# Kernel optimization log

Hardware: AMD Instinct MI355X
Metric: run time of the kernel (lower is better)

Reference implementation:

```python
import jax, jax.numpy as jnp
import numpy as np

# e3nn normalize2mom gain for tanh (1/sqrt(E[tanh(z)^2]), z~N(0,1))
TANH_GAIN = 1.5927116870880127
B, M_IN, M_HID, M_OUT = 8192, 64, 128, 64

_W_SPECS = {
    'b1_l1_w0': (64, 64), 'b1_l1_w1': (64, 64), 'b1_l2_w0': (64, 64), 'b1_l2_w1': (64, 64),
    'b1_tp_ss': (64, 64, 128), 'b1_tp_vv': (64, 64, 128), 'b1_tp_sv': (64, 64, 128), 'b1_tp_vs': (64, 64, 128),
    'b1_g_ws': (128, 128), 'b1_g_wg': (128, 128), 'b1_g_wv': (128, 128),
    'b1_o_w0': (128, 128), 'b1_o_w1': (128, 128),
    'b2_l1_w0': (128, 128), 'b2_l1_w1': (128, 128), 'b2_l2_w0': (128, 128), 'b2_l2_w1': (128, 128),
    'b2_tp_ss': (128, 128, 128), 'b2_tp_vv': (128, 128, 128), 'b2_tp_sv': (128, 128, 128), 'b2_tp_vs': (128, 128, 128),
    'b2_g_ws': (128, 128), 'b2_g_wg': (128, 128), 'b2_g_wv': (128, 128),
    'b2_o_w0': (128, 128), 'b2_o_w1': (128, 128),
    'f_w0': (128, 64), 'f_w1': (128, 64),
}


def setup_inputs() -> dict:
    key = jax.random.key(0)
    ks = jax.random.split(key, len(_W_SPECS) + 1)
    d = {'x': jax.random.normal(ks[0], (B, M_IN + 3 * M_IN), jnp.float32)}
    for i, (name, shp) in enumerate(_W_SPECS.items()):
        d[name] = jax.random.normal(ks[i + 1], shp, jnp.float32)  # e3nn weights ~ N(0,1)
    return d


def _lin(s, v, w0, w1):
    # o3.Linear on 'Mx0e+Mx1o': per-irrep block matmul, path_normalization='element' -> 1/sqrt(fan_in)
    c = 1.0 / np.sqrt(w0.shape[0])
    return (s @ w0) * c, jnp.einsum('bui,uw->bwi', v, w1) * c


def _tp(s1, v1, s2, v2, wss, wvv, wsv, wvs):
    # FullyConnectedTensorProduct, irrep_normalization='component', path_normalization='element'.
    # Two uvw paths feed each output irrep -> path_weight = sqrt(dim_out / (2*M*M)).
    # CG values: w3j(0,0,0)=1; w3j(0,1,1)=delta/sqrt(3); w3j(1,0,1)=delta/sqrt(3); w3j(1,1,0)=delta/sqrt(3).
    M = s1.shape[-1]
    c = 1.0 / (M * np.sqrt(2.0))
    s = c * jnp.einsum('bu,bv,uvw->bw', s1, s2, wss) \
        + (c / np.sqrt(3.0)) * jnp.einsum('bui,bvi,uvw->bw', v1, v2, wvv)
    v = c * (jnp.einsum('bu,bvi,uvw->bwi', s1, v2, wsv)
             + jnp.einsum('bui,bv,uvw->bwi', v1, s2, wvs))
    return s, v


def _gate(s, v, ws, wg, wv):
    # LearnableGate: o3.Linear to (scalars | gate scalars | vectors), then e3nn Gate
    # (tanh w/ normalize2mom gain on scalars and gates; elementwise gate*vector has unit path weight).
    c = 1.0 / np.sqrt(ws.shape[0])
    sl = (s @ ws) * c
    g = (s @ wg) * c
    vl = jnp.einsum('bui,uw->bwi', v, wv) * c
    return TANH_GAIN * jnp.tanh(sl), (TANH_GAIN * jnp.tanh(g))[..., None] * vl


def _block(s, v, p):
    l1w0, l1w1, l2w0, l2w1, wss, wvv, wsv, wvs, gws, gwg, gwv, ow0, ow1 = p
    s1, v1 = _lin(s, v, l1w0, l1w1)
    s2, v2 = _lin(s, v, l2w0, l2w1)
    s, v = _tp(s1, v1, s2, v2, wss, wvv, wsv, wvs)
    s, v = _gate(s, v, gws, gwg, gwv)
    return _lin(s, v, ow0, ow1)


def _forward(x, *w):
    s = x[:, :M_IN]
    v = x[:, M_IN:].reshape(x.shape[0], M_IN, 3)
    s, v = _block(s, v, w[0:13])
    s, v = _block(s, v, w[13:26])
    s, v = _lin(s, v, w[26], w[27])
    return jnp.concatenate([s, v.reshape(v.shape[0], -1)], axis=-1)


def reference(x, b1_l1_w0, b1_l1_w1, b1_l2_w0, b1_l2_w1, b1_tp_ss, b1_tp_vv, b1_tp_sv, b1_tp_vs, b1_g_ws, b1_g_wg, b1_g_wv, b1_o_w0, b1_o_w1, b2_l1_w0, b2_l1_w1, b2_l2_w0, b2_l2_w1, b2_tp_ss, b2_tp_vv, b2_tp_sv, b2_tp_vs, b2_g_ws, b2_g_wg, b2_g_wv, b2_o_w0, b2_o_w1, f_w0, f_w1):
    return _forward(x, b1_l1_w0, b1_l1_w1, b1_l2_w0, b1_l2_w1, b1_tp_ss, b1_tp_vv, b1_tp_sv, b1_tp_vs, b1_g_ws, b1_g_wg, b1_g_wv, b1_o_w0, b1_o_w1, b2_l1_w0, b2_l1_w1, b2_l2_w0, b2_l2_w1, b2_tp_ss, b2_tp_vv, b2_tp_sv, b2_tp_vs, b2_g_ws, b2_g_wg, b2_g_wv, b2_o_w0, b2_o_w1, f_w0, f_w1)
```

## Files before the change

kernel.cpp:

```cpp
#include <hip/hip_runtime.h>
#include <math.h>

typedef _Float16 f16;
typedef __attribute__((ext_vector_type(8))) _Float16 half8;
typedef __attribute__((ext_vector_type(4))) _Float16 half4;
typedef __attribute__((ext_vector_type(4))) float floatx4;

#define NB 8192

struct ConvJob { const float* src; f16* dst; int K; int N; int ucount; float scale; int swz; };
struct ConvJobs { ConvJob j[28]; };

__global__ void convert_w(ConvJobs JJ) {
    ConvJob jb = JJ.j[blockIdx.z];
    int u = blockIdx.x;
    if (u >= jb.ucount) return;
    __shared__ f16 tile[128 * 136];
    const int K = jb.K, N = jb.N;
    const int npad = N + 8;
    const int nsh = (N == 128) ? 7 : 6;
    const int ksh = (K == 128) ? 7 : 6;
    const float* src = jb.src + (size_t)u * K * N;
    for (int idx = threadIdx.x; idx < K * N; idx += 256) {
        int k = idx >> nsh, n = idx & (N - 1);
        tile[k * npad + n] = (f16)(src[idx] * jb.scale);
    }
    __syncthreads();
    f16* dst = jb.dst + (size_t)u * N * K;
    for (int idx = threadIdx.x; idx < N * K; idx += 256) {
        int n = idx >> ksh, rem = idx & (K - 1);
        int g2 = rem >> 3, jj = rem & 7;
        int g = jb.swz ? (g2 ^ (n & jb.swz)) : g2;
        int k = g * 8 + jj;
        dst[idx] = tile[k * npad + n];
    }
}

__global__ void x_to_planes(const float* __restrict__ x, f16* s_p, f16* v0, f16* v1, f16* v2) {
    int t = blockIdx.x * 256 + threadIdx.x;
    if (t >= NB * 64) return;
    int b = t >> 6, u = t & 63;
    const float* xr = x + (size_t)b * 256;
    s_p[t] = (f16)xr[u];
    v0[t] = (f16)xr[64 + 3 * u + 0];
    v1[t] = (f16)xr[64 + 3 * u + 1];
    v2[t] = (f16)xr[64 + 3 * u + 2];
}

struct TpJob { const f16* p; const f16* q; const f16* w; float* out; int pstride; int qstride; };
struct TpJobs { TpJob j[10]; };

template <int M>
__launch_bounds__(256, (M == 128) ? 3 : 4)
__global__ void tp_unit(TpJobs JJ) {
    TpJob jb = JJ.j[blockIdx.z];
    constexpr int KC = M / 32;
    constexpr int GPR = M / 8;
    constexpr int GM = GPR - 1;
    constexpr int SLABH = 64 * M;
    constexpr int PIECES = SLABH / 8;
    constexpr int IPW = PIECES / 256;
    constexpr int SLABFULL = 128 * M;
    __shared__ f16 w_lds[2][SLABH];
    const int tid = threadIdx.x, lane = tid & 63, wave = tid >> 6;
    const int wm = wave & 1, wn = wave >> 1;
    const int l15 = lane & 15, quad = lane >> 4;
    const int rowBase = blockIdx.x * 128;
    const int colBase = blockIdx.y * 64;

    half8 qf[4][KC];
    int prow[4];
    #pragma unroll
    for (int t = 0; t < 4; t++) {
        int row = rowBase + wm * 64 + t * 16 + l15;
        prow[t] = row;
        const f16* qr = jb.q + (size_t)row * jb.qstride;
        #pragma unroll
        for (int c = 0; c < KC; c++) qf[t][c] = *(const half8*)(qr + c * 32 + quad * 8);
    }
    floatx4 acc[4][2];
    #pragma unroll
    for (int a = 0; a < 4; a++)
        #pragma unroll
        for (int b = 0; b < 2; b++) acc[a][b] = (floatx4){0.f, 0.f, 0.f, 0.f};

    int rd_off[2][KC];
    #pragma unroll
    for (int nt = 0; nt < 2; nt++) {
        int nl = wn * 32 + nt * 16 + l15;
        #pragma unroll
        for (int c = 0; c < KC; c++) {
            int g = c * 4 + quad;
            rd_off[nt][c] = nl * M + ((g ^ (nl & GM)) << 3);
        }
    }

    const int wpBase = wave * (PIECES / 4);
    const f16* wsrc0 = jb.w + (size_t)colBase * M + (size_t)(wpBase + lane) * 8;
    f16* ldst0 = &w_lds[0][0] + (size_t)wpBase * 8;
    f16* ldst1 = &w_lds[1][0] + (size_t)wpBase * 8;
    auto stage = [&](int u, int buf) {
        const f16* src = wsrc0 + (size_t)u * SLABFULL;
        f16* dst = buf ? ldst1 : ldst0;
        #pragma unroll
        for (int i = 0; i < IPW; i++) {
            __builtin_amdgcn_global_load_lds(
                (const __attribute__((address_space(1))) void*)(src + i * 64 * 8),
                (__attribute__((address_space(3))) void*)(dst + i * 64 * 8),
                16, 0, 0);
        }
    };

    stage(0, 0);
    __syncthreads();

    for (int uc = 0; uc < M / 8; uc++) {
        half8 pcur[4];
        #pragma unroll
        for (int t = 0; t < 4; t++)
            pcur[t] = *(const half8*)(jb.p + (size_t)prow[t] * jb.pstride + uc * 8);
        #pragma unroll
        for (int j = 0; j < 8; j++) {
            const int u = uc * 8 + j;
            const int cur = j & 1;
            if (j != 7 || uc != M / 8 - 1) stage(u + 1, cur ^ 1);
            #pragma unroll
            for (int c = 0; c < KC; c++) {
                half8 af[4];
                #pragma unroll
                for (int t = 0; t < 4; t++) {
                    f16 pv = pcur[t][j];
                    half8 p8 = {pv, pv, pv, pv, pv, pv, pv, pv};
                    af[t] = qf[t][c] * p8;
                }
                #pragma unroll
                for (int nt = 0; nt < 2; nt++) {
                    half8 bf = *(const half8*)&w_lds[cur][rd_off[nt][c]];
                    #pragma unroll
                    for (int t = 0; t < 4; t++)
                        acc[t][nt] = __builtin_amdgcn_mfma_f32_16x16x32_f16(af[t], bf, acc[t][nt], 0, 0, 0);
                }
            }
            __syncthreads();
        }
    }
    #pragma unroll
    for (int t = 0; t < 4; t++)
        #pragma unroll
        for (int nt = 0; nt < 2; nt++) {
            int col = colBase + wn * 32 + nt * 16 + l15;
            float* orow = jb.out + (size_t)(rowBase + wm * 64 + t * 16 + quad * 4) * 128 + col;
            #pragma unroll
            for (int r = 0; r < 4; r++) orow[(size_t)r * 128] = acc[t][nt][r];
        }
}

struct SmallJob { const f16* A; const f16* W; char* out; int astride; int ostride;
                  int ocol; int cstride; int mode; int Njob; int ny;
                  const f16* Amul; int mstride; };
struct SmallJobs { SmallJob j[4]; };

template <int K>
__launch_bounds__(256, 2)
__global__ void small_gemm(SmallJobs JJ) {
    SmallJob jb = JJ.j[blockIdx.z];
    if ((int)blockIdx.y >= jb.ny) return;
    constexpr int KC = K / 32;
    constexpr int NP = K + 8;
    constexpr int PR = K / 8;
    constexpr int PPT = 128 * K / 8 / 256;
    __shared__ f16 w_lds[128 * NP];
    const int tid = threadIdx.x, lane = tid & 63, wave = tid >> 6;
    const int wm = wave & 1, wn = wave >> 1;
    const int l15 = lane & 15, quad = lane >> 4;
    const int rowBase = blockIdx.x * 128;
    const int nBase = blockIdx.y * 128;

    #pragma unroll
    for (int t = 0; t < PPT; t++) {
        int idx = t * 256 + tid;
        int r = idx / PR, pc = idx % PR;
        int4 v = {0, 0, 0, 0};
        if (nBase + r < jb.Njob)
            v = *(const int4*)(jb.W + (size_t)(nBase + r) * K + pc * 8);
        *(int4*)&w_lds[r * NP + pc * 8] = v;
    }
    half8 qf[4][KC];
    for (int t = 0; t < 4; t++) {
        int row = rowBase + wm * 64 + t * 16 + l15;
        const f16* ar = jb.A + (size_t)row * jb.astride;
        #pragma unroll
        for (int c = 0; c < KC; c++) qf[t][c] = *(const half8*)(ar + c * 32 + quad * 8);
        if (jb.Amul) {
            const f16* mr = jb.Amul + (size_t)row * jb.mstride;
            #pragma unroll
            for (int c = 0; c < KC; c++) qf[t][c] = qf[t][c] * *(const half8*)(mr + c * 32 + quad * 8);
        }
    }
    floatx4 acc[4][4];
    #pragma unroll
    for (int a = 0; a < 4; a++)
        #pragma unroll
        for (int b = 0; b < 4; b++) acc[a][b] = (floatx4){0.f, 0.f, 0.f, 0.f};
    __syncthreads();
    #pragma unroll
    for (int c = 0; c < KC; c++)
        #pragma unroll
        for (int nt = 0; nt < 4; nt++) {
            half8 bf = *(const half8*)&w_lds[(wn * 64 + nt * 16 + l15) * NP + c * 32 + quad * 8];
            #pragma unroll
            for (int t = 0; t < 4; t++)
                acc[t][nt] = __builtin_amdgcn_mfma_f32_16x16x32_f16(qf[t][c], bf, acc[t][nt], 0, 0, 0);
        }
    const float GAIN = 1.5927116870880127f;
    #pragma unroll
    for (int t = 0; t < 4; t++)
        #pragma unroll
        for (int nt = 0; nt < 4; nt++) {
            int col = nBase + wn * 64 + nt * 16 + l15;
            if (col >= jb.Njob) continue;
            int rowB = rowBase + wm * 64 + t * 16 + quad * 4;
            #pragma unroll
            for (int r = 0; r < 4; r++) {
                float v = acc[t][nt][r];
                size_t ro = (size_t)(rowB + r) * jb.ostride;
                if (jb.mode == 0)      ((f16*)jb.out)[ro + jb.ocol + col] = (f16)v;
                else if (jb.mode == 1) ((f16*)jb.out)[ro + jb.ocol + col] = (f16)(GAIN * tanhf(v));
                else                   ((float*)jb.out)[ro + jb.ocol + (size_t)col * jb.cstride] = v;
            }
        }
}

__global__ void tp_reduce(const float4* __restrict__ P, half4* s_tp, half4* v0, half4* v1, half4* v2) {
    int t = blockIdx.x * 256 + threadIdx.x;
    if (t >= NB * 32) return;
    const size_t S = (size_t)NB * 32;
    float4 a0 = P[t], a1 = P[S + t], a2 = P[2 * S + t], a3 = P[3 * S + t];
    float4 b0 = P[4 * S + t], b1 = P[5 * S + t], b2 = P[6 * S + t];
    float4 c0 = P[7 * S + t], c1 = P[8 * S + t], c2 = P[9 * S + t];
    s_tp[t] = (half4){(f16)(a0.x + a1.x + a2.x + a3.x), (f16)(a0.y + a1.y + a2.y + a3.y),
                      (f16)(a0.z + a1.z + a2.z + a3.z), (f16)(a0.w + a1.w + a2.w + a3.w)};
    v0[t] = (half4){(f16)(b0.x + c0.x), (f16)(b0.y + c0.y), (f16)(b0.z + c0.z), (f16)(b0.w + c0.w)};
    v1[t] = (half4){(f16)(b1.x + c1.x), (f16)(b1.y + c1.y), (f16)(b1.z + c1.z), (f16)(b1.w + c1.w)};
    v2[t] = (half4){(f16)(b2.x + c2.x), (f16)(b2.y + c2.y), (f16)(b2.z + c2.z), (f16)(b2.w + c2.w)};
}

extern "C" void kernel_launch(void* const* d_in, const int* in_sizes, int n_in,
                              void* d_out, int out_size, void* d_ws, size_t ws_size,
                              hipStream_t stream) {
    const float* x = (const float*)d_in[0];
    const float* W_IN[28];
    for (int i = 0; i < 28; i++) W_IN[i] = (const float*)d_in[1 + i];

    char* base = (char*)d_ws;
    size_t off = 0;
    auto alloc = [&](size_t bytes) -> char* {
        char* p = base + off;
        off += (bytes + 255) & ~(size_t)255;
        return p;
    };
    const size_t S128 = (size_t)NB * 128;

    f16* Wl12_b1_s = (f16*)alloc(8192 * 2);
    f16* Wl12_b1_v = (f16*)alloc(8192 * 2);
    f16* Wl12_b2_s = (f16*)alloc(32768 * 2);
    f16* Wl12_b2_v = (f16*)alloc(32768 * 2);
    f16* Wtp_b1[4]; for (int i = 0; i < 4; i++) Wtp_b1[i] = (f16*)alloc((size_t)64 * 128 * 64 * 2);
    f16* Wtp_b2[4]; for (int i = 0; i < 4; i++) Wtp_b2[i] = (f16*)alloc((size_t)128 * 128 * 128 * 2);
    f16* Wg_b1_sg = (f16*)alloc(32768 * 2);
    f16* Wg_b1_v  = (f16*)alloc(16384 * 2);
    f16* Wg_b2_sg = (f16*)alloc(32768 * 2);
    f16* Wg_b2_v  = (f16*)alloc(16384 * 2);
    f16* Wo_b1_s = (f16*)alloc(16384 * 2);
    f16* Wo_b1_v = (f16*)alloc(16384 * 2);
    f16* Wo_b2_s = (f16*)alloc(16384 * 2);
    f16* Wo_b2_v = (f16*)alloc(16384 * 2);
    f16* Wf_s = (f16*)alloc(8192 * 2);
    f16* Wf_v = (f16*)alloc(8192 * 2);
    f16* s_p = (f16*)alloc((size_t)NB * 64 * 2);
    f16* v_p[3]; for (int i = 0; i < 3; i++) v_p[i] = (f16*)alloc((size_t)NB * 64 * 2);
    f16* Breg = (f16*)alloc((size_t)4 * NB * 256 * 2);
    float* Part = (float*)alloc((size_t)10 * S128 * 4);
    f16* Dreg = (f16*)alloc((size_t)4 * S128 * 2);
    f16* Ereg = (f16*)alloc((size_t)5 * S128 * 2);
    f16* Freg = (f16*)alloc((size_t)4 * S128 * 2);
    (void)ws_size; (void)in_sizes; (void)n_in; (void)out_size;

    const float c_l1 = 0.125f;
    const float c128 = 0.088388347648318447f;
    const float c1 = 1.0f / (64.0f * 1.4142135623730951f);
    const float c2 = 1.0f / (128.0f * 1.4142135623730951f);
    const float i3 = 0.57735026918962584f;

    ConvJobs CJ;
    int jn = 0;
    auto CV = [&](const float* s, f16* d, int K, int N, int uc, float sc, int swz) {
        CJ.j[jn++] = ConvJob{s, d, K, N, uc, sc, swz};
    };
    CV(W_IN[0], Wl12_b1_s, 64, 64, 1, c_l1, 0);  CV(W_IN[2], Wl12_b1_s + 4096, 64, 64, 1, c_l1, 0);
    CV(W_IN[1], Wl12_b1_v, 64, 64, 1, c_l1, 0);  CV(W_IN[3], Wl12_b1_v + 4096, 64, 64, 1, c_l1, 0);
    CV(W_IN[13], Wl12_b2_s, 128, 128, 1, c128, 0); CV(W_IN[15], Wl12_b2_s + 16384, 128, 128, 1, c128, 0);
    CV(W_IN[14], Wl12_b2_v, 128, 128, 1, c128, 0); CV(W_IN[16], Wl12_b2_v + 16384, 128, 128, 1, c128, 0);
    CV(W_IN[4], Wtp_b1[0], 64, 128, 64, c1, 7);  CV(W_IN[5], Wtp_b1[1], 64, 128, 64, c1 * i3, 7);
    CV(W_IN[6], Wtp_b1[2], 64, 128, 64, c1, 7);  CV(W_IN[7], Wtp_b1[3], 64, 128, 64, c1, 7);
    CV(W_IN[17], Wtp_b2[0], 128, 128, 128, c2, 15); CV(W_IN[18], Wtp_b2[1], 128, 128, 128, c2 * i3, 15);
    CV(W_IN[19], Wtp_b2[2], 128, 128, 128, c2, 15); CV(W_IN[20], Wtp_b2[3], 128, 128, 128, c2, 15);
    CV(W_IN[8], Wg_b1_sg, 128, 128, 1, c128, 0);  CV(W_IN[9], Wg_b1_sg + 16384, 128, 128, 1, c128, 0);
    CV(W_IN[10], Wg_b1_v, 128, 128, 1, c128, 0);
    CV(W_IN[21], Wg_b2_sg, 128, 128, 1, c128, 0); CV(W_IN[22], Wg_b2_sg + 16384, 128, 128, 1, c128, 0);
    CV(W_IN[23], Wg_b2_v, 128, 128, 1, c128, 0);
    CV(W_IN[11], Wo_b1_s, 128, 128, 1, c128, 0);  CV(W_IN[12], Wo_b1_v, 128, 128, 1, c128, 0);
    CV(W_IN[24], Wo_b2_s, 128, 128, 1, c128, 0);  CV(W_IN[25], Wo_b2_v, 128, 128, 1, c128, 0);
    CV(W_IN[26], Wf_s, 128, 64, 1, c128, 0);      CV(W_IN[27], Wf_v, 128, 64, 1, c128, 0);
    convert_w<<<dim3(128, 1, 28), 256, 0, stream>>>(CJ);

    x_to_planes<<<NB * 64 / 256, 256, 0, stream>>>(x, s_p, v_p[0], v_p[1], v_p[2]);

    auto SJ = [](const f16* A, const f16* W, void* out, int as, int os, int oc, int cs,
                 int mode, int Nj, int ny, const f16* Amul, int ms) {
        return SmallJob{A, W, (char*)out, as, os, oc, cs, mode, Nj, ny, Amul, ms};
    };

    f16* s12 = Breg;
    f16* v12[3]; for (int i = 0; i < 3; i++) v12[i] = Breg + (size_t)(1 + i) * NB * 128;
    f16* s_tp = Dreg; f16* v_tp[3]; for (int i = 0; i < 3; i++) v_tp[i] = Dreg + (1 + i) * S128;
    f16* sg_gg = Ereg;
    f16* vl[3]; for (int i = 0; i < 3; i++) vl[i] = Ereg + 2 * S128 + i * S128;
    f16* s_o = Freg; f16* v_o[3]; for (int i = 0; i < 3; i++) v_o[i] = Freg + (1 + i) * S128;

    {
        SmallJobs J;
        J.j[0] = SJ(s_p, Wl12_b1_s, s12, 64, 128, 0, 1, 0, 128, 1, nullptr, 0);
        for (int i = 0; i < 3; i++) J.j[1 + i] = SJ(v_p[i], Wl12_b1_v, v12[i], 64, 128, 0, 1, 0, 128, 1, nullptr, 0);
        small_gemm<64><<<dim3(64, 1, 4), 256, 0, stream>>>(J);
    }
    {
        TpJobs J;
        J.j[0] = TpJob{s12, s12 + 64, Wtp_b1[0], Part + 0 * S128, 128, 128};
        for (int i = 0; i < 3; i++) J.j[1 + i] = TpJob{v12[i], v12[i] + 64, Wtp_b1[1], Part + (1 + i) * S128, 128, 128};
        for (int i = 0; i < 3; i++) J.j[4 + i] = TpJob{s12, v12[i] + 64, Wtp_b1[2], Part + (4 + i) * S128, 128, 128};
        for (int i = 0; i < 3; i++) J.j[7 + i] = TpJob{v12[i], s12 + 64, Wtp_b1[3], Part + (7 + i) * S128, 128, 128};
        tp_unit<64><<<dim3(64, 2, 10), 256, 0, stream>>>(J);
    }
    tp_reduce<<<NB * 32 / 256, 256, 0, stream>>>((const float4*)Part, (half4*)s_tp, (half4*)v_tp[0], (half4*)v_tp[1], (half4*)v_tp[2]);
    {
        SmallJobs J;
        J.j[0] = SJ(s_tp, Wg_b1_sg, sg_gg, 128, 256, 0, 1, 1, 256, 2, nullptr, 0);
        for (int i = 0; i < 3; i++) J.j[1 + i] = SJ(v_tp[i], Wg_b1_v, vl[i], 128, 128, 0, 1, 0, 128, 1, nullptr, 0);
        small_gemm<128><<<dim3(64, 2, 4), 256, 0, stream>>>(J);
    }
    {
        SmallJobs J;
        J.j[0] = SJ(sg_gg, Wo_b1_s, s_o, 256, 128, 0, 1, 0, 128, 1, nullptr, 0);
        for (int i = 0; i < 3; i++) J.j[1 + i] = SJ(vl[i], Wo_b1_v, v_o[i], 128, 128, 0, 1, 0, 128, 1, sg_gg + 128, 256);
        small_gemm<128><<<dim3(64, 1, 4), 256, 0, stream>>>(J);
    }
    f16* s12b = Breg;
    f16* v12b[3]; for (int i = 0; i < 3; i++) v12b[i] = Breg + (size_t)(1 + i) * NB * 256;
    {
        SmallJobs J;
        J.j[0] = SJ(s_o, Wl12_b2_s, s12b, 128, 256, 0, 1, 0, 256, 2, nullptr, 0);
        for (int i = 0; i < 3; i++) J.j[1 + i] = SJ(v_o[i], Wl12_b2_v, v12b[i], 128, 256, 0, 1, 0, 256, 2, nullptr, 0);
        small_gemm<128><<<dim3(64, 2, 4), 256, 0, stream>>>(J);
    }
    {
        TpJobs J;
        J.j[0] = TpJob{s12b, s12b + 128, Wtp_b2[0], Part + 0 * S128, 256, 256};
        for (int i = 0; i < 3; i++) J.j[1 + i] = TpJob{v12b[i], v12b[i] + 128, Wtp_b2[1], Part + (1 + i) * S128, 256, 256};
        for (int i = 0; i < 3; i++) J.j[4 + i] = TpJob{s12b, v12b[i] + 128, Wtp_b2[2], Part + (4 + i) * S128, 256, 256};
        for (int i = 0; i < 3; i++) J.j[7 + i] = TpJob{v12b[i], s12b + 128, Wtp_b2[3], Part + (7 + i) * S128, 256, 256};
        tp_unit<128><<<dim3(64, 2, 10), 256, 0, stream>>>(J);
    }
    tp_reduce<<<NB * 32 / 256, 256, 0, stream>>>((const float4*)Part, (half4*)s_tp, (half4*)v_tp[0], (half4*)v_tp[1], (half4*)v_tp[2]);
    {
        SmallJobs J;
        J.j[0] = SJ(s_tp, Wg_b2_sg, sg_gg, 128, 256, 0, 1, 1, 256, 2, nullptr, 0);
        for (int i = 0; i < 3; i++) J.j[1 + i] = SJ(v_tp[i], Wg_b2_v, vl[i], 128, 128, 0, 1, 0, 128, 1, nullptr, 0);
        small_gemm<128><<<dim3(64, 2, 4), 256, 0, stream>>>(J);
    }
    {
        SmallJobs J;
        J.j[0] = SJ(sg_gg, Wo_b2_s, s_o, 256, 128, 0, 1, 0, 128, 1, nullptr, 0);
        for (int i = 0; i < 3; i++) J.j[1 + i] = SJ(vl[i], Wo_b2_v, v_o[i], 128, 128, 0, 1, 0, 128, 1, sg_gg + 128, 256);
        small_gemm<128><<<dim3(64, 1, 4), 256, 0, stream>>>(J);
    }
    {
        SmallJobs J;
        J.j[0] = SJ(s_o, Wf_s, d_out, 128, 256, 0, 1, 2, 64, 1, nullptr, 0);
        for (int i = 0; i < 3; i++) J.j[1 + i] = SJ(v_o[i], Wf_v, d_out, 128, 256, 64 + i, 3, 2, 64, 1, nullptr, 0);
        small_gemm<128><<<dim3(64, 1, 4), 256, 0, stream>>>(J);
    }
}
```

Before: 638.3 us.

## Triple-buffer TP weight staging and fuse partial reduction into gate GEMM

The tensor-product kernel moves from double to triple LDS buffering. It prefetches two slabs ahead and replaces __syncthreads with a partial vmcnt wait plus barrier, so global-to-LDS loads can overlap compute. The separate tp_reduce kernel is removed, and the gate small_gemm now sums the fp32 partials directly while loading its A operand. This saves one launch and an fp16 intermediate round trip per block. In exchange the triple buffer raises LDS use, which may reduce occupancy for M=128, and the y=2 gate GEMM blocks re-read the fp32 partials redundantly.

```diff
diff --git a/kernel.cpp b/kernel.cpp
--- a/kernel.cpp
+++ b/kernel.cpp
@@ -61,7 +61,7 @@
     constexpr int PIECES = SLABH / 8;
     constexpr int IPW = PIECES / 256;
     constexpr int SLABFULL = 128 * M;
-    __shared__ f16 w_lds[2][SLABH];
+    __shared__ f16 w_lds[3][SLABH];
     const int tid = threadIdx.x, lane = tid & 63, wave = tid >> 6;
     const int wm = wave & 1, wn = wave >> 1;
     const int l15 = lane & 15, quad = lane >> 4;
@@ -97,11 +97,9 @@
 
     const int wpBase = wave * (PIECES / 4);
     const f16* wsrc0 = jb.w + (size_t)colBase * M + (size_t)(wpBase + lane) * 8;
-    f16* ldst0 = &w_lds[0][0] + (size_t)wpBase * 8;
-    f16* ldst1 = &w_lds[1][0] + (size_t)wpBase * 8;
     auto stage = [&](int u, int buf) {
         const f16* src = wsrc0 + (size_t)u * SLABFULL;
-        f16* dst = buf ? ldst1 : ldst0;
+        f16* dst = &w_lds[buf][0] + (size_t)wpBase * 8;
         #pragma unroll
         for (int i = 0; i < IPW; i++) {
             __builtin_amdgcn_global_load_lds(
@@ -112,8 +110,10 @@
     };
 
     stage(0, 0);
-    __syncthreads();
-
+    stage(1, 1);
+    __asm__ __volatile__("s_waitcnt vmcnt(%0)\n\ts_barrier" :: "n"(IPW) : "memory");
+
+    int ib = 0;
     for (int uc = 0; uc < M / 8; uc++) {
         half8 pcur[4];
         #pragma unroll
@@ -122,8 +122,9 @@
         #pragma unroll
         for (int j = 0; j < 8; j++) {
             const int u = uc * 8 + j;
-            const int cur = j & 1;
-            if (j != 7 || uc != M / 8 - 1) stage(u + 1, cur ^ 1);
+            int unext = u + 2; if (unext > M - 1) unext = M - 1;
+            int is = ib + 2; if (is >= 3) is -= 3;
+            stage(unext, is);
             #pragma unroll
             for (int c = 0; c < KC; c++) {
                 half8 af[4];
@@ -135,13 +136,14 @@
                 }
                 #pragma unroll
                 for (int nt = 0; nt < 2; nt++) {
-                    half8 bf = *(const half8*)&w_lds[cur][rd_off[nt][c]];
+                    half8 bf = *(const half8*)&w_lds[ib][rd_off[nt][c]];
                     #pragma unroll
                     for (int t = 0; t < 4; t++)
                         acc[t][nt] = __builtin_amdgcn_mfma_f32_16x16x32_f16(af[t], bf, acc[t][nt], 0, 0, 0);
                 }
             }
-            __syncthreads();
+            __asm__ __volatile__("s_waitcnt vmcnt(%0)\n\ts_barrier" :: "n"(IPW) : "memory");
+            ib = ib + 1; if (ib == 3) ib = 0;
         }
     }
     #pragma unroll
@@ -157,7 +159,9 @@
 
 struct SmallJob { const f16* A; const f16* W; char* out; int astride; int ostride;
                   int ocol; int cstride; int mode; int Njob; int ny;
-                  const f16* Amul; int mstride; };
+                  const f16* Amul; int mstride;
+                  const float* red0; const float* red1; const float* red2; const float* red3;
+                  int nred; };
 struct SmallJobs { SmallJob j[4]; };
 
 template <int K>
@@ -188,9 +192,23 @@
     half8 qf[4][KC];
     for (int t = 0; t < 4; t++) {
         int row = rowBase + wm * 64 + t * 16 + l15;
-        const f16* ar = jb.A + (size_t)row * jb.astride;
-        #pragma unroll
-        for (int c = 0; c < KC; c++) qf[t][c] = *(const half8*)(ar + c * 32 + quad * 8);
+        if (jb.nred) {
+            #pragma unroll
+            for (int c = 0; c < KC; c++) {
+                size_t boff = (size_t)row * 128 + c * 32 + quad * 8;
+                floatx4 s0 = *(const floatx4*)(jb.red0 + boff);
+                floatx4 s1 = *(const floatx4*)(jb.red0 + boff + 4);
+                if (jb.nred > 1) { s0 += *(const floatx4*)(jb.red1 + boff); s1 += *(const floatx4*)(jb.red1 + boff + 4); }
+                if (jb.nred > 2) { s0 += *(const floatx4*)(jb.red2 + boff); s1 += *(const floatx4*)(jb.red2 + boff + 4); }
+                if (jb.nred > 3) { s0 += *(const floatx4*)(jb.red3 + boff); s1 += *(const floatx4*)(jb.red3 + boff + 4); }
+                qf[t][c] = (half8){(f16)s0.x, (f16)s0.y, (f16)s0.z, (f16)s0.w,
+                                   (f16)s1.x, (f16)s1.y, (f16)s1.z, (f16)s1.w};
+            }
+        } else {
+            const f16* ar = jb.A + (size_t)row * jb.astride;
+            #pragma unroll
+            for (int c = 0; c < KC; c++) qf[t][c] = *(const half8*)(ar + c * 32 + quad * 8);
+        }
         if (jb.Amul) {
             const f16* mr = jb.Amul + (size_t)row * jb.mstride;
             #pragma unroll
@@ -229,20 +247,6 @@
                 else                   ((float*)jb.out)[ro + jb.ocol + (size_t)col * jb.cstride] = v;
             }
         }
-}
-
-__global__ void tp_reduce(const float4* __restrict__ P, half4* s_tp, half4* v0, half4* v1, half4* v2) {
-    int t = blockIdx.x * 256 + threadIdx.x;
-    if (t >= NB * 32) return;
-    const size_t S = (size_t)NB * 32;
-    float4 a0 = P[t], a1 = P[S + t], a2 = P[2 * S + t], a3 = P[3 * S + t];
-    float4 b0 = P[4 * S + t], b1 = P[5 * S + t], b2 = P[6 * S + t];
-    float4 c0 = P[7 * S + t], c1 = P[8 * S + t], c2 = P[9 * S + t];
-    s_tp[t] = (half4){(f16)(a0.x + a1.x + a2.x + a3.x), (f16)(a0.y + a1.y + a2.y + a3.y),
-                      (f16)(a0.z + a1.z + a2.z + a3.z), (f16)(a0.w + a1.w + a2.w + a3.w)};
-    v0[t] = (half4){(f16)(b0.x + c0.x), (f16)(b0.y + c0.y), (f16)(b0.z + c0.z), (f16)(b0.w + c0.w)};
-    v1[t] = (half4){(f16)(b1.x + c1.x), (f16)(b1.y + c1.y), (f16)(b1.z + c1.z), (f16)(b1.w + c1.w)};
-    v2[t] = (half4){(f16)(b2.x + c2.x), (f16)(b2.y + c2.y), (f16)(b2.z + c2.z), (f16)(b2.w + c2.w)};
 }
 
 extern "C" void kernel_launch(void* const* d_in, const int* in_sizes, int n_in,
@@ -281,7 +285,6 @@
     f16* v_p[3]; for (int i = 0; i < 3; i++) v_p[i] = (f16*)alloc((size_t)NB * 64 * 2);
     f16* Breg = (f16*)alloc((size_t)4 * NB * 256 * 2);
     float* Part = (float*)alloc((size_t)10 * S128 * 4);
-    f16* Dreg = (f16*)alloc((size_t)4 * S128 * 2);
     f16* Ereg = (f16*)alloc((size_t)5 * S128 * 2);
     f16* Freg = (f16*)alloc((size_t)4 * S128 * 2);
     (void)ws_size; (void)in_sizes; (void)n_in; (void)out_size;
@@ -318,12 +321,12 @@
 
     auto SJ = [](const f16* A, const f16* W, void* out, int as, int os, int oc, int cs,
                  int mode, int Nj, int ny, const f16* Amul, int ms) {
-        return SmallJob{A, W, (char*)out, as, os, oc, cs, mode, Nj, ny, Amul, ms};
+        return SmallJob{A, W, (char*)out, as, os, oc, cs, mode, Nj, ny, Amul, ms,
+                        nullptr, nullptr, nullptr, nullptr, 0};
     };
 
     f16* s12 = Breg;
     f16* v12[3]; for (int i = 0; i < 3; i++) v12[i] = Breg + (size_t)(1 + i) * NB * 128;
-    f16* s_tp = Dreg; f16* v_tp[3]; for (int i = 0; i < 3; i++) v_tp[i] = Dreg + (1 + i) * S128;
     f16* sg_gg = Ereg;
     f16* vl[3]; for (int i = 0; i < 3; i++) vl[i] = Ereg + 2 * S128 + i * S128;
     f16* s_o = Freg; f16* v_o[3]; for (int i = 0; i < 3; i++) v_o[i] = Freg + (1 + i) * S128;
@@ -342,11 +345,13 @@
         for (int i = 0; i < 3; i++) J.j[7 + i] = TpJob{v12[i], s12 + 64, Wtp_b1[3], Part + (7 + i) * S128, 128, 128};
         tp_unit<64><<<dim3(64, 2, 10), 256, 0, stream>>>(J);
     }
-    tp_reduce<<<NB * 32 / 256, 256, 0, stream>>>((const float4*)Part, (half4*)s_tp, (half4*)v_tp[0], (half4*)v_tp[1], (half4*)v_tp[2]);
-    {
-        SmallJobs J;
-        J.j[0] = SJ(s_tp, Wg_b1_sg, sg_gg, 128, 256, 0, 1, 1, 256, 2, nullptr, 0);
-        for (int i = 0; i < 3; i++) J.j[1 + i] = SJ(v_tp[i], Wg_b1_v, vl[i], 128, 128, 0, 1, 0, 128, 1, nullptr, 0);
+    {
+        SmallJobs J;
+        J.j[0] = SmallJob{nullptr, Wg_b1_sg, (char*)sg_gg, 128, 256, 0, 1, 1, 256, 2, nullptr, 0,
+                          Part + 0 * S128, Part + 1 * S128, Part + 2 * S128, Part + 3 * S128, 4};
+        for (int i = 0; i < 3; i++)
+            J.j[1 + i] = SmallJob{nullptr, Wg_b1_v, (char*)vl[i], 128, 128, 0, 1, 0, 128, 1, nullptr, 0,
+                                  Part + (4 + i) * S128, Part + (7 + i) * S128, nullptr, nullptr, 2};
         small_gemm<128><<<dim3(64, 2, 4), 256, 0, stream>>>(J);
     }
     {
@@ -371,11 +376,13 @@
         for (int i = 0; i < 3; i++) J.j[7 + i] = TpJob{v12b[i], s12b + 128, Wtp_b2[3], Part + (7 + i) * S128, 256, 256};
         tp_unit<128><<<dim3(64, 2, 10), 256, 0, stream>>>(J);
     }
-    tp_reduce<<<NB * 32 / 256, 256, 0, stream>>>((const float4*)Part, (half4*)s_tp, (half4*)v_tp[0], (half4*)v_tp[1], (half4*)v_tp[2]);
-    {
-        SmallJobs J;
-        J.j[0] = SJ(s_tp, Wg_b2_sg, sg_gg, 128, 256, 0, 1, 1, 256, 2, nullptr, 0);
-        for (int i = 0; i < 3; i++) J.j[1 + i] = SJ(v_tp[i], Wg_b2_v, vl[i], 128, 128, 0, 1, 0, 128, 1, nullptr, 0);
+    {
+        SmallJobs J;
+        J.j[0] = SmallJob{nullptr, Wg_b2_sg, (char*)sg_gg, 128, 256, 0, 1, 1, 256, 2, nullptr, 0,
+                          Part + 0 * S128, Part + 1 * S128, Part + 2 * S128, Part + 3 * S128, 4};
+        for (int i = 0; i < 3; i++)
+            J.j[1 + i] = SmallJob{nullptr, Wg_b2_v, (char*)vl[i], 128, 128, 0, 1, 0, 128, 1, nullptr, 0,
+                                  Part + (4 + i) * S128, Part + (7 + i) * S128, nullptr, nullptr, 2};
         small_gemm<128><<<dim3(64, 2, 4), 256, 0, stream>>>(J);
     }
     {
```

After: 703.0 us. 10.1% more time.

## Share weight slabs across three planes per TP block and pre-sum vv paths

Applied to the files above, without the earlier changes.

Restructures the tensor-product kernel so each block processes three row planes (the three vector components, or three row chunks for the ss path) against one staged weight slab. This reuses each LDS weight slab three times instead of once and cuts redundant weight traffic. The vv path sums its three components in registers before storing, which shrinks the partial buffer from ten to eight planes and reduces tp_reduce reads. It raises register pressure, lowers occupancy through launch bounds, and adds clamped rows and early exits for the ss job's uneven row tiling.

```diff
diff --git a/kernel.cpp b/kernel.cpp
--- a/kernel.cpp
+++ b/kernel.cpp
@@ -47,16 +47,18 @@
     v2[t] = (f16)xr[64 + 3 * u + 2];
 }
 
-struct TpJob { const f16* p; const f16* q; const f16* w; float* out; int pstride; int qstride; };
-struct TpJobs { TpJob j[10]; };
+struct Tp3Job { const f16* q0; const f16* q1; const f16* q2;
+                const f16* p0; const f16* p1; const f16* p2;
+                const f16* w; float* o0; float* o1; float* o2;
+                int qs; int ps; int rowmul; int rowadd; int sum; };
+struct Tp3Jobs { Tp3Job j[4]; };
 
 template <int M>
-__launch_bounds__(256, (M == 128) ? 3 : 4)
-__global__ void tp_unit(TpJobs JJ) {
-    TpJob jb = JJ.j[blockIdx.z];
+__launch_bounds__(256, (M == 128) ? 2 : 3)
+__global__ void tp3(Tp3Jobs JJ) {
+    Tp3Job jb = JJ.j[blockIdx.z];
     constexpr int KC = M / 32;
-    constexpr int GPR = M / 8;
-    constexpr int GM = GPR - 1;
+    constexpr int GM = M / 8 - 1;
     constexpr int SLABH = 64 * M;
     constexpr int PIECES = SLABH / 8;
     constexpr int IPW = PIECES / 256;
@@ -65,24 +67,34 @@
     const int tid = threadIdx.x, lane = tid & 63, wave = tid >> 6;
     const int wm = wave & 1, wn = wave >> 1;
     const int l15 = lane & 15, quad = lane >> 4;
-    const int rowBase = blockIdx.x * 128;
+    const int bx = blockIdx.x;
+    if (jb.rowmul == 192 && bx * 192 >= NB) return;
     const int colBase = blockIdx.y * 64;
 
-    half8 qf[4][KC];
-    int prow[4];
-    #pragma unroll
-    for (int t = 0; t < 4; t++) {
-        int row = rowBase + wm * 64 + t * 16 + l15;
-        prow[t] = row;
-        const f16* qr = jb.q + (size_t)row * jb.qstride;
-        #pragma unroll
-        for (int c = 0; c < KC; c++) qf[t][c] = *(const half8*)(qr + c * 32 + quad * 8);
-    }
-    floatx4 acc[4][2];
-    #pragma unroll
-    for (int a = 0; a < 4; a++)
-        #pragma unroll
-        for (int b = 0; b < 2; b++) acc[a][b] = (floatx4){0.f, 0.f, 0.f, 0.f};
+    const f16* qptr[3] = {jb.q0, jb.q1, jb.q2};
+    const f16* pptr[3] = {jb.p0, jb.p1, jb.p2};
+    float* optr[3] = {jb.o0, jb.o1, jb.o2};
+
+    int prow[3][2];
+    half8 qf[3][2][KC];
+    #pragma unroll
+    for (int pl = 0; pl < 3; pl++)
+        #pragma unroll
+        for (int mt = 0; mt < 2; mt++) {
+            int row = bx * jb.rowmul + pl * jb.rowadd + wm * 32 + mt * 16 + l15;
+            if (row >= NB) row = NB - 1;
+            prow[pl][mt] = row;
+            const f16* qr = qptr[pl] + (size_t)row * jb.qs;
+            #pragma unroll
+            for (int c = 0; c < KC; c++) qf[pl][mt][c] = *(const half8*)(qr + c * 32 + quad * 8);
+        }
+    floatx4 acc[3][2][2];
+    #pragma unroll
+    for (int pl = 0; pl < 3; pl++)
+        #pragma unroll
+        for (int a = 0; a < 2; a++)
+            #pragma unroll
+            for (int b = 0; b < 2; b++) acc[pl][a][b] = (floatx4){0.f, 0.f, 0.f, 0.f};
 
     int rd_off[2][KC];
     #pragma unroll
@@ -97,11 +109,9 @@
 
     const int wpBase = wave * (PIECES / 4);
     const f16* wsrc0 = jb.w + (size_t)colBase * M + (size_t)(wpBase + lane) * 8;
-    f16* ldst0 = &w_lds[0][0] + (size_t)wpBase * 8;
-    f16* ldst1 = &w_lds[1][0] + (size_t)wpBase * 8;
     auto stage = [&](int u, int buf) {
         const f16* src = wsrc0 + (size_t)u * SLABFULL;
-        f16* dst = buf ? ldst1 : ldst0;
+        f16* dst = &w_lds[buf][0] + (size_t)wpBase * 8;
         #pragma unroll
         for (int i = 0; i < IPW; i++) {
             __builtin_amdgcn_global_load_lds(
@@ -115,10 +125,12 @@
     __syncthreads();
 
     for (int uc = 0; uc < M / 8; uc++) {
-        half8 pcur[4];
-        #pragma unroll
-        for (int t = 0; t < 4; t++)
-            pcur[t] = *(const half8*)(jb.p + (size_t)prow[t] * jb.pstride + uc * 8);
+        half8 pcur[3][2];
+        #pragma unroll
+        for (int pl = 0; pl < 3; pl++)
+            #pragma unroll
+            for (int mt = 0; mt < 2; mt++)
+                pcur[pl][mt] = *(const half8*)(pptr[pl] + (size_t)prow[pl][mt] * jb.ps + uc * 8);
         #pragma unroll
         for (int j = 0; j < 8; j++) {
             const int u = uc * 8 + j;
@@ -126,33 +138,56 @@
             if (j != 7 || uc != M / 8 - 1) stage(u + 1, cur ^ 1);
             #pragma unroll
             for (int c = 0; c < KC; c++) {
-                half8 af[4];
+                half8 bf[2];
                 #pragma unroll
-                for (int t = 0; t < 4; t++) {
-                    f16 pv = pcur[t][j];
-                    half8 p8 = {pv, pv, pv, pv, pv, pv, pv, pv};
-                    af[t] = qf[t][c] * p8;
-                }
+                for (int nt = 0; nt < 2; nt++)
+                    bf[nt] = *(const half8*)&w_lds[cur][rd_off[nt][c]];
                 #pragma unroll
-                for (int nt = 0; nt < 2; nt++) {
-                    half8 bf = *(const half8*)&w_lds[cur][rd_off[nt][c]];
+                for (int pl = 0; pl < 3; pl++) {
+                    half8 af[2];
                     #pragma unroll
-                    for (int t = 0; t < 4; t++)
-                        acc[t][nt] = __builtin_amdgcn_mfma_f32_16x16x32_f16(af[t], bf, acc[t][nt], 0, 0, 0);
+                    for (int mt = 0; mt < 2; mt++) {
+                        f16 pv = pcur[pl][mt][j];
+                        half8 p8 = {pv, pv, pv, pv, pv, pv, pv, pv};
+                        af[mt] = qf[pl][mt][c] * p8;
+                    }
+                    #pragma unroll
+                    for (int nt = 0; nt < 2; nt++)
+                        #pragma unroll
+                        for (int mt = 0; mt < 2; mt++)
+                            acc[pl][mt][nt] = __builtin_amdgcn_mfma_f32_16x16x32_f16(af[mt], bf[nt], acc[pl][mt][nt], 0, 0, 0);
                 }
             }
             __syncthreads();
         }
     }
-    #pragma unroll
-    for (int t = 0; t < 4; t++)
-        #pragma unroll
-        for (int nt = 0; nt < 2; nt++) {
-            int col = colBase + wn * 32 + nt * 16 + l15;
-            float* orow = jb.out + (size_t)(rowBase + wm * 64 + t * 16 + quad * 4) * 128 + col;
-            #pragma unroll
-            for (int r = 0; r < 4; r++) orow[(size_t)r * 128] = acc[t][nt][r];
-        }
+    if (jb.sum) {
+        #pragma unroll
+        for (int mt = 0; mt < 2; mt++)
+            #pragma unroll
+            for (int nt = 0; nt < 2; nt++) {
+                floatx4 a = acc[0][mt][nt] + acc[1][mt][nt] + acc[2][mt][nt];
+                int col = colBase + wn * 32 + nt * 16 + l15;
+                int rowB = bx * 64 + wm * 32 + mt * 16 + quad * 4;
+                float* orow = jb.o0 + (size_t)rowB * 128 + col;
+                #pragma unroll
+                for (int r = 0; r < 4; r++) orow[(size_t)r * 128] = a[r];
+            }
+    } else {
+        #pragma unroll
+        for (int pl = 0; pl < 3; pl++)
+            #pragma unroll
+            for (int mt = 0; mt < 2; mt++)
+                #pragma unroll
+                for (int nt = 0; nt < 2; nt++) {
+                    int col = colBase + wn * 32 + nt * 16 + l15;
+                    int rowB = bx * jb.rowmul + pl * jb.rowadd + wm * 32 + mt * 16 + quad * 4;
+                    if (rowB >= NB) continue;
+                    float* orow = optr[pl] + (size_t)rowB * 128 + col;
+                    #pragma unroll
+                    for (int r = 0; r < 4; r++) orow[(size_t)r * 128] = acc[pl][mt][nt][r];
+                }
+    }
 }
 
 struct SmallJob { const f16* A; const f16* W; char* out; int astride; int ostride;
@@ -235,11 +270,11 @@
     int t = blockIdx.x * 256 + threadIdx.x;
     if (t >= NB * 32) return;
     const size_t S = (size_t)NB * 32;
-    float4 a0 = P[t], a1 = P[S + t], a2 = P[2 * S + t], a3 = P[3 * S + t];
-    float4 b0 = P[4 * S + t], b1 = P[5 * S + t], b2 = P[6 * S + t];
-    float4 c0 = P[7 * S + t], c1 = P[8 * S + t], c2 = P[9 * S + t];
-    s_tp[t] = (half4){(f16)(a0.x + a1.x + a2.x + a3.x), (f16)(a0.y + a1.y + a2.y + a3.y),
-                      (f16)(a0.z + a1.z + a2.z + a3.z), (f16)(a0.w + a1.w + a2.w + a3.w)};
+    float4 a0 = P[t], a1 = P[S + t];
+    float4 b0 = P[2 * S + t], b1 = P[3 * S + t], b2 = P[4 * S + t];
+    float4 c0 = P[5 * S + t], c1 = P[6 * S + t], c2 = P[7 * S + t];
+    s_tp[t] = (half4){(f16)(a0.x + a1.x), (f16)(a0.y + a1.y),
+                      (f16)(a0.z + a1.z), (f16)(a0.w + a1.w)};
     v0[t] = (half4){(f16)(b0.x + c0.x), (f16)(b0.y + c0.y), (f16)(b0.z + c0.z), (f16)(b0.w + c0.w)};
     v1[t] = (half4){(f16)(b1.x + c1.x), (f16)(b1.y + c1.y), (f16)(b1.z + c1.z), (f16)(b1.w + c1.w)};
     v2[t] = (half4){(f16)(b2.x + c2.x), (f16)(b2.y + c2.y), (f16)(b2.z + c2.z), (f16)(b2.w + c2.w)};
@@ -280,7 +315,7 @@
     f16* s_p = (f16*)alloc((size_t)NB * 64 * 2);
     f16* v_p[3]; for (int i = 0; i < 3; i++) v_p[i] = (f16*)alloc((size_t)NB * 64 * 2);
     f16* Breg = (f16*)alloc((size_t)4 * NB * 256 * 2);
-    float* Part = (float*)alloc((size_t)10 * S128 * 4);
+    float* Part = (float*)alloc((size_t)8 * S128 * 4);
     f16* Dreg = (f16*)alloc((size_t)4 * S128 * 2);
     f16* Ereg = (f16*)alloc((size_t)5 * S128 * 2);
     f16* Freg = (f16*)alloc((size_t)4 * S128 * 2);
@@ -320,6 +355,28 @@
                  int mode, int Nj, int ny, const f16* Amul, int ms) {
         return SmallJob{A, W, (char*)out, as, os, oc, cs, mode, Nj, ny, Amul, ms};
     };
+    auto tp_jobs = [&](f16* s12p, f16* v12p0, f16* v12p1, f16* v12p2, f16* Wtp[4],
+                       int M, int stride) {
+        f16* v12p[3] = {v12p0, v12p1, v12p2};
+        Tp3Jobs J;
+        J.j[0] = Tp3Job{v12p[0] + M, v12p[1] + M, v12p[2] + M,
+                        v12p[0], v12p[1], v12p[2],
+                        Wtp[1], Part + 1 * S128, Part + 1 * S128, Part + 1 * S128,
+                        stride, stride, 64, 0, 1};
+        J.j[1] = Tp3Job{v12p[0] + M, v12p[1] + M, v12p[2] + M,
+                        s12p, s12p, s12p,
+                        Wtp[2], Part + 2 * S128, Part + 3 * S128, Part + 4 * S128,
+                        stride, stride, 64, 0, 0};
+        J.j[2] = Tp3Job{s12p + M, s12p + M, s12p + M,
+                        v12p[0], v12p[1], v12p[2],
+                        Wtp[3], Part + 5 * S128, Part + 6 * S128, Part + 7 * S128,
+                        stride, stride, 64, 0, 0};
+        J.j[3] = Tp3Job{s12p + M, s12p + M, s12p + M,
+                        s12p, s12p, s12p,
+                        Wtp[0], Part + 0 * S128, Part + 0 * S128, Part + 0 * S128,
+                        stride, stride, 192, 64, 0};
+        return J;
+    };
 
     f16* s12 = Breg;
     f16* v12[3]; for (int i = 0; i < 3; i++) v12[i] = Breg + (size_t)(1 + i) * NB * 128;
@@ -335,12 +392,8 @@
         small_gemm<64><<<dim3(64, 1, 4), 256, 0, stream>>>(J);
     }
     {
-        TpJobs J;
-        J.j[0] = TpJob{s12, s12 + 64, Wtp_b1[0], Part + 0 * S128, 128, 128};
-        for (int i = 0; i < 3; i++) J.j[1 + i] = TpJob{v12[i], v12[i] + 64, Wtp_b1[1], Part + (1 + i) * S128, 128, 128};
-        for (int i = 0; i < 3; i++) J.j[4 + i] = TpJob{s12, v12[i] + 64, Wtp_b1[2], Part + (4 + i) * S128, 128, 128};
-        for (int i = 0; i < 3; i++) J.j[7 + i] = TpJob{v12[i], s12 + 64, Wtp_b1[3], Part + (7 + i) * S128, 128, 128};
-        tp_unit<64><<<dim3(64, 2, 10), 256, 0, stream>>>(J);
+        Tp3Jobs J = tp_jobs(s12, v12[0], v12[1], v12[2], Wtp_b1, 64, 128);
+        tp3<64><<<dim3(128, 2, 4), 256, 0, stream>>>(J);
     }
     tp_reduce<<<NB * 32 / 256, 256, 0, stream>>>((const float4*)Part, (half4*)s_tp, (half4*)v_tp[0], (half4*)v_tp[1], (half4*)v_tp[2]);
     {
@@ -364,12 +417,8 @@
         small_gemm<128><<<dim3(64, 2, 4), 256, 0, stream>>>(J);
     }
     {
-        TpJobs J;
-        J.j[0] = TpJob{s12b, s12b + 128, Wtp_b2[0], Part + 0 * S128, 256, 256};
-        for (int i = 0; i < 3; i++) J.j[1 + i] = TpJob{v12b[i], v12b[i] + 128, Wtp_b2[1], Part + (1 + i) * S128, 256, 256};
-        for (int i = 0; i < 3; i++) J.j[4 + i] = TpJob{s12b, v12b[i] + 128, Wtp_b2[2], Part + (4 + i) * S128, 256, 256};
-        for (int i = 0; i < 3; i++) J.j[7 + i] = TpJob{v12b[i], s12b + 128, Wtp_b2[3], Part + (7 + i) * S128, 256, 256};
-        tp_unit<128><<<dim3(64, 2, 10), 256, 0, stream>>>(J);
+        Tp3Jobs J = tp_jobs(s12b, v12b[0], v12b[1], v12b[2], Wtp_b2, 128, 256);
+        tp3<128><<<dim3(128, 2, 4), 256, 0, stream>>>(J);
     }
     tp_reduce<<<NB * 32 / 256, 256, 0, stream>>>((const float4*)Part, (half4*)s_tp, (half4*)v_tp[0], (half4*)v_tp[1], (half4*)v_tp[2]);
     {
```

Result: slower. 687.5 us (+7.7%).
